# Kernel tuning notes

Hardware: AMD Instinct MI355X
Metric: run time of the kernel (lower is better)

The kernel has to match this reference:

```python
import jax, jax.numpy as jnp
import numpy as np

B, L, DM, DIN, N, R, K, H = 4, 2048, 1024, 2048, 16, 64, 4, 1024
EPS = 1e-5


def setup_inputs() -> dict:
    key = jax.random.key(0)
    ks = jax.random.split(key, 12)
    nrm = lambda k, shp, s=0.02: jax.random.normal(k, shp, jnp.float32) * s
    return dict(
        hidden_states=jax.random.normal(ks[0], (B, L, DM), jnp.float32),
        residual=jax.random.normal(ks[1], (B, L, DM), jnp.float32),
        norm_w=jnp.ones((DM,), jnp.float32),
        in_proj_w=nrm(ks[2], (2 * DIN, DM)),
        conv_w=nrm(ks[3], (DIN, K), 0.2),
        conv_b=jnp.zeros((DIN,), jnp.float32),
        x_proj_w=nrm(ks[4], (R + 2 * N, DIN)),
        dt_proj_w=nrm(ks[5], (DIN, R), 0.1),
        dt_proj_b=jnp.log(jnp.expm1(jnp.full((DIN,), 0.01, jnp.float32))),
        A_log=jnp.log(jnp.tile(jnp.arange(1, N + 1, dtype=jnp.float32), (DIN, 1))),
        D=jnp.ones((DIN,), jnp.float32),
        out_proj_w=nrm(ks[6], (DM, DIN)),
        norm2_w=jnp.ones((DM,), jnp.float32),
        fc1_w=nrm(ks[7], (2 * H, DM)),
        fc2_w=nrm(ks[8], (DM, H)),
    )


def _rmsnorm(x, w):
    return x * jax.lax.rsqrt(jnp.mean(x * x, axis=-1, keepdims=True) + EPS) * w


def _mixer(h, in_proj_w, conv_w, conv_b, x_proj_w, dt_proj_w, dt_proj_b,
           A_log, D, out_proj_w):
    # in_proj -> x, z : (B, L, DIN) each
    xz = jnp.einsum('bld,ed->ble', h, in_proj_w)
    x, z = jnp.split(xz, 2, axis=-1)
    # depthwise causal conv along L
    xc = x.transpose(0, 2, 1)  # (B, DIN, L)
    xc = jax.lax.conv_general_dilated(
        xc, conv_w[:, None, :], window_strides=(1,), padding=[(K - 1, 0)],
        feature_group_count=DIN)
    xc = xc + conv_b[None, :, None]
    x = jax.nn.silu(xc).transpose(0, 2, 1)  # (B, L, DIN)
    # x_proj -> dt_low, B, C
    dbl = jnp.einsum('bld,ed->ble', x, x_proj_w)
    dt_low, Bm, Cm = jnp.split(dbl, [R, R + N], axis=-1)
    dt = jax.nn.softplus(jnp.einsum('blr,dr->bld', dt_low, dt_proj_w) + dt_proj_b)
    A = -jnp.exp(A_log)  # (DIN, N)

    def step(hc, inp):
        dt_t, B_t, C_t, x_t = inp  # (B,DIN),(B,N),(B,N),(B,DIN)
        hc = jnp.exp(dt_t[..., None] * A) * hc + (dt_t * x_t)[..., None] * B_t[:, None, :]
        return hc, jnp.einsum('bdn,bn->bd', hc, C_t)

    h0 = jnp.zeros((B, DIN, N), x.dtype)
    _, ys = jax.lax.scan(step, h0, (dt.transpose(1, 0, 2), Bm.transpose(1, 0, 2),
                                    Cm.transpose(1, 0, 2), x.transpose(1, 0, 2)))
    y = ys.transpose(1, 0, 2) + x * D  # skip term D*u
    y = y * jax.nn.silu(z)
    return jnp.einsum('bld,ed->ble', y, out_proj_w)


def reference(hidden_states, residual, norm_w, in_proj_w, conv_w, conv_b,
              x_proj_w, dt_proj_w, dt_proj_b, A_log, D, out_proj_w,
              norm2_w, fc1_w, fc2_w):
    # pre-norm residual path (fused_add_norm=False, residual_in_fp32=True)
    res = hidden_states + residual
    hn = _rmsnorm(res, norm_w)
    mix = _mixer(hn, in_proj_w, conv_w, conv_b, x_proj_w, dt_proj_w,
                 dt_proj_b, A_log, D, out_proj_w)
    # NOTE: faithful to source: residual is overwritten by norm2(mix+res),
    # while mlp is applied to the raw mixer output.
    res2 = _rmsnorm(mix + res, norm2_w)
    fc = jnp.einsum('bld,hd->blh', mix, fc1_w)
    y, gate = jnp.split(fc, 2, axis=-1)
    out = jnp.einsum('blh,dh->bld', y * jax.nn.silu(gate), fc2_w)
    return (out, res2)
```

## Files before the change

### kernel.cpp

```cpp
#include <hip/hip_runtime.h>
#include <hip/hip_bf16.h>

#define B_   4
#define L_   2048
#define DM_  1024
#define DIN_ 2048
#define NS_  16
#define R_   64
#define KC_  4
#define H_   1024
#define BL_  (B_ * L_)
#define CCH  32
#define CHL  (L_ / CCH)

typedef __attribute__((ext_vector_type(4))) float f32x4;
typedef __attribute__((ext_vector_type(8))) short bf16x8;
typedef __attribute__((ext_vector_type(8))) unsigned short u16x8;

__device__ __forceinline__ float b2f(unsigned short u) {
    union { unsigned int i; float f; } v; v.i = ((unsigned int)u) << 16; return v.f;
}
__device__ __forceinline__ unsigned short f2b(float f) {
    union { float f; unsigned int i; } v; v.f = f;
    unsigned int r = v.i + 0x7fffu + ((v.i >> 16) & 1u);
    return (unsigned short)(r >> 16);
}
__device__ __forceinline__ float sigmoidf_(float x) { return 1.f / (1.f + __expf(-x)); }
__device__ __forceinline__ float softplusf_(float x) { return (x > 20.f) ? x : log1pf(__expf(x)); }

__device__ __forceinline__ void gload16(const unsigned short* g, unsigned short* l) {
    __builtin_amdgcn_global_load_lds(
        (__attribute__((address_space(1))) void*)(g),
        (__attribute__((address_space(3))) void*)(l), 16, 0, 0);
}

__global__ void k_cvt(const float* __restrict__ in, unsigned short* __restrict__ out, int n) {
    int i = blockIdx.x * blockDim.x + threadIdx.x;
    if (i < n) out[i] = f2b(in[i]);
}
__global__ void k_fill0(unsigned short* __restrict__ out, int n) {
    int i = blockIdx.x * blockDim.x + threadIdx.x;
    if (i < n) out[i] = 0;
}

__global__ __launch_bounds__(256)
void k_reduceX(const float* __restrict__ part, unsigned short* __restrict__ dblB,
               float* __restrict__ dblF) {
    int i = blockIdx.x * 256 + threadIdx.x;
    if (i >= BL_ * 96) return;
    int r = i / 96, n = i - r * 96;
    const float* p = part + (size_t)r * 2048;
    float s = p[n] + p[128 + n] + p[256 + n] + p[384 + n];
    dblB[(size_t)r * 96 + n] = f2b(s);
    if (n >= 64) dblF[(size_t)r * 32 + n - 64] = s;
}

__global__ __launch_bounds__(256)
void k_add_rmsnorm(const float* __restrict__ a, const float* __restrict__ b,
                   const float* __restrict__ w,
                   float* __restrict__ resOut, unsigned short* __restrict__ hnOut) {
    int row = blockIdx.x, tid = threadIdx.x;
    const float4* ap = (const float4*)(a + (size_t)row * DM_);
    const float4* bp = (const float4*)(b + (size_t)row * DM_);
    float4 va = ap[tid], vb = bp[tid];
    float4 s = make_float4(va.x + vb.x, va.y + vb.y, va.z + vb.z, va.w + vb.w);
    ((float4*)(resOut + (size_t)row * DM_))[tid] = s;
    float ss = s.x * s.x + s.y * s.y + s.z * s.z + s.w * s.w;
    #pragma unroll
    for (int m = 32; m >= 1; m >>= 1) ss += __shfl_xor(ss, m);
    __shared__ float red[4];
    if ((tid & 63) == 0) red[tid >> 6] = ss;
    __syncthreads();
    float tot = red[0] + red[1] + red[2] + red[3];
    float sc = rsqrtf(tot / (float)DM_ + 1e-5f);
    float4 vw = ((const float4*)w)[tid];
    unsigned short* hp = hnOut + (size_t)row * DM_ + tid * 4;
    *(ushort4*)hp = make_ushort4(f2b(s.x * sc * vw.x), f2b(s.y * sc * vw.y),
                                 f2b(s.z * sc * vw.z), f2b(s.w * sc * vw.w));
}

__global__ __launch_bounds__(256)
void k_add_rmsnorm2(const float* __restrict__ mix, const float* __restrict__ res,
                    const float* __restrict__ w,
                    float* __restrict__ res2Out, unsigned short* __restrict__ mixB) {
    int row = blockIdx.x, tid = threadIdx.x;
    const float4* mp = (const float4*)(mix + (size_t)row * DM_);
    const float4* rp = (const float4*)(res + (size_t)row * DM_);
    float4 vm = mp[tid], vr = rp[tid];
    float4 s = make_float4(vm.x + vr.x, vm.y + vr.y, vm.z + vr.z, vm.w + vr.w);
    unsigned short* mb = mixB + (size_t)row * DM_ + tid * 4;
    *(ushort4*)mb = make_ushort4(f2b(vm.x), f2b(vm.y), f2b(vm.z), f2b(vm.w));
    float ss = s.x * s.x + s.y * s.y + s.z * s.z + s.w * s.w;
    #pragma unroll
    for (int m = 32; m >= 1; m >>= 1) ss += __shfl_xor(ss, m);
    __shared__ float red[4];
    if ((tid & 63) == 0) red[tid >> 6] = ss;
    __syncthreads();
    float tot = red[0] + red[1] + red[2] + red[3];
    float sc = rsqrtf(tot / (float)DM_ + 1e-5f);
    float4 vw = ((const float4*)w)[tid];
    float4 o = make_float4(s.x * sc * vw.x, s.y * sc * vw.y, s.z * sc * vw.z, s.w * sc * vw.w);
    ((float4*)(res2Out + (size_t)row * DM_))[tid] = o;
}

__global__ __launch_bounds__(256)
void k_conv_silu(const unsigned short* __restrict__ xz,
                 const float* __restrict__ cw, const float* __restrict__ cb,
                 unsigned short* __restrict__ xc) {
    const int tid = threadIdx.x;
    const int d0 = tid * 8;
    const int b  = blockIdx.x >> 8;
    const int t0 = (blockIdx.x & 255) * 8;
    const unsigned short* xbase = xz + (size_t)b * L_ * (2 * DIN_) + d0;
    unsigned short* obase = xc + (size_t)b * L_ * DIN_ + d0;

    float4 w[8];
    float bias[8];
    #pragma unroll
    for (int j = 0; j < 8; j++) {
        w[j] = ((const float4*)cw)[d0 + j];
        bias[j] = cb[d0 + j];
    }
    u16x8 zero = (u16x8){0, 0, 0, 0, 0, 0, 0, 0};
    u16x8 r0 = zero, r1 = zero, r2 = zero, r3;
    if (t0 >= 3) {
        r0 = *(const u16x8*)(xbase + (size_t)(t0 - 3) * (2 * DIN_));
        r1 = *(const u16x8*)(xbase + (size_t)(t0 - 2) * (2 * DIN_));
        r2 = *(const u16x8*)(xbase + (size_t)(t0 - 1) * (2 * DIN_));
    }
    #pragma unroll
    for (int tt = 0; tt < 8; tt++) {
        int t = t0 + tt;
        r3 = *(const u16x8*)(xbase + (size_t)t * (2 * DIN_));
        u16x8 out;
        #pragma unroll
        for (int j = 0; j < 8; j++) {
            float acc = bias[j] + w[j].x * b2f(r0[j]) + w[j].y * b2f(r1[j])
                                + w[j].z * b2f(r2[j]) + w[j].w * b2f(r3[j]);
            out[j] = f2b(acc * sigmoidf_(acc));
        }
        *(u16x8*)(obase + (size_t)t * DIN_) = out;
        r0 = r1; r1 = r2; r2 = r3;
    }
}

__global__ void k_gate(const unsigned short* __restrict__ fc, unsigned short* __restrict__ g) {
    int i = blockIdx.x * blockDim.x + threadIdx.x;
    if (i >= BL_ * H_) return;
    int h = i % H_;
    int row = i / H_;
    float y = b2f(fc[(size_t)row * (2 * H_) + h]);
    float gt = b2f(fc[(size_t)row * (2 * H_) + H_ + h]);
    g[i] = f2b(y * gt * sigmoidf_(gt));
}

__global__ __launch_bounds__(256)
void k_scan_p1(const unsigned short* __restrict__ dty, const unsigned short* __restrict__ xc,
               const float* __restrict__ dblF, const float* __restrict__ A_log,
               unsigned short* __restrict__ Q, unsigned short* __restrict__ sumdt) {
    const int tid = threadIdx.x;
    const int d = (blockIdx.x & 7) * 256 + tid;
    const int b = blockIdx.x >> 3;
    const int c = blockIdx.y;
    const int t0 = c * CHL;

    float a[NS_], h[NS_];
    #pragma unroll
    for (int n = 0; n < NS_; n++) { a[n] = -__expf(A_log[d * NS_ + n]); h[n] = 0.f; }
    float sd = 0.f;

    const unsigned short* dp  = dty + (size_t)b * L_ * DIN_ + d;
    const unsigned short* xp  = xc  + (size_t)b * L_ * DIN_ + d;
    const float* bcp = dblF + (size_t)(b * L_ + t0) * 32;

    #pragma unroll 2
    for (int t = 0; t < CHL; t++) {
        int tg = t0 + t;
        float dtv = b2f(dp[(size_t)tg * DIN_]);
        float xv  = b2f(xp[(size_t)tg * DIN_]);
        sd += dtv;
        float bx = dtv * xv;
        const float* bc = bcp + t * 32;
        #pragma unroll
        for (int n = 0; n < NS_; n++)
            h[n] = __expf(dtv * a[n]) * h[n] + bx * bc[n];
    }
    unsigned short* q = Q + ((size_t)(b * CCH + c) * DIN_ + d) * NS_;
    u16x8 qa, qb;
    #pragma unroll
    for (int j = 0; j < 8; j++) { qa[j] = f2b(h[j]); qb[j] = f2b(h[8 + j]); }
    *(u16x8*)q = qa;
    *(u16x8*)(q + 8) = qb;
    sumdt[(size_t)(b * CCH + c) * DIN_ + d] = f2b(sd);
}

__global__ __launch_bounds__(256)
void k_scan_comb(unsigned short* __restrict__ Q, const unsigned short* __restrict__ sumdt,
                 const float* __restrict__ A_log) {
    int i = blockIdx.x * 256 + threadIdx.x;
    int n = i & 15;
    int d = (i >> 4) & (DIN_ - 1);
    int b = i >> 15;
    float a = -__expf(A_log[d * NS_ + n]);
    float h = 0.f;
    for (int c = 0; c < CCH; c++) {
        size_t base = ((size_t)(b * CCH + c) * DIN_ + d);
        float q  = b2f(Q[base * NS_ + n]);
        float sd = b2f(sumdt[base]);
        if (c > 0) Q[((size_t)(b * CCH + c - 1) * DIN_ + d) * NS_ + n] = f2b(h);
        h = __expf(a * sd) * h + q;
    }
}

__global__ __launch_bounds__(256)
void k_scan_p3(unsigned short* __restrict__ dty, const unsigned short* __restrict__ xc,
               const float* __restrict__ dblF, const float* __restrict__ A_log,
               const float* __restrict__ Dp, const unsigned short* __restrict__ xz,
               const unsigned short* __restrict__ Qh) {
    const int tid = threadIdx.x;
    const int d = (blockIdx.x & 7) * 256 + tid;
    const int b = blockIdx.x >> 3;
    const int c = blockIdx.y;
    const int t0 = c * CHL;

    float a[NS_], h[NS_];
    #pragma unroll
    for (int n = 0; n < NS_; n++) a[n] = -__expf(A_log[d * NS_ + n]);
    if (c == 0) {
        #pragma unroll
        for (int n = 0; n < NS_; n++) h[n] = 0.f;
    } else {
        const unsigned short* qh = Qh + ((size_t)(b * CCH + c - 1) * DIN_ + d) * NS_;
        u16x8 v0 = *(const u16x8*)qh;
        u16x8 v1 = *(const u16x8*)(qh + 8);
        #pragma unroll
        for (int j = 0; j < 8; j++) { h[j] = b2f(v0[j]); h[8 + j] = b2f(v1[j]); }
    }
    float Dd = Dp[d];

    unsigned short* dp = dty + (size_t)b * L_ * DIN_ + d;
    const unsigned short* xp  = xc + (size_t)b * L_ * DIN_ + d;
    const unsigned short* zp  = xz + (size_t)b * L_ * (2 * DIN_) + DIN_ + d;
    const float* bcp = dblF + (size_t)(b * L_ + t0) * 32;

    #pragma unroll 2
    for (int t = 0; t < CHL; t++) {
        int tg = t0 + t;
        float dtv = b2f(dp[(size_t)tg * DIN_]);
        float xv  = b2f(xp[(size_t)tg * DIN_]);
        float bx = dtv * xv;
        const float* bc = bcp + t * 32;
        float y = 0.f;
        #pragma unroll
        for (int n = 0; n < NS_; n++) {
            h[n] = __expf(dtv * a[n]) * h[n] + bx * bc[n];
            y += h[n] * bc[16 + n];
        }
        y += xv * Dd;
        float zv = b2f(zp[(size_t)tg * (2 * DIN_)]);
        dp[(size_t)tg * DIN_] = f2b(y * zv * sigmoidf_(zv));
    }
}

template <int EPI, int SPLITK = 0>
__global__ __launch_bounds__(256)
void k_gemm(const unsigned short* __restrict__ A, int lda,
            const unsigned short* __restrict__ Bw, int ldb,
            void* __restrict__ outp, int ldc, const float* __restrict__ bias,
            int M, int N, int Kd, int Nstore) {
    if constexpr (SPLITK) {
        const int z = blockIdx.z;
        A += (size_t)z * 512;
        Bw += (size_t)z * 512;
        outp = (void*)((float*)outp + z * 128);
    }
    __shared__ unsigned short As[128 * 32];
    __shared__ unsigned short Bs[128 * 32];
    const int tid = threadIdx.x;
    const int lane = tid & 63;
    const int w = tid >> 6;
    const int wr = w >> 1, wc = w & 1;
    const int bm = blockIdx.y * 128, bn = blockIdx.x * 128;

    const int e0 = tid * 8;
    const int r0 = e0 >> 5;
    const int c0 = e0 & 31;
    const int r1 = r0 + 64;

    f32x4 acc[4][4];
    #pragma unroll
    for (int i = 0; i < 4; i++)
        #pragma unroll
        for (int j = 0; j < 4; j++) acc[i][j] = (f32x4){0.f, 0.f, 0.f, 0.f};

    const int fr = lane & 15, ko = (lane >> 4) * 8;

    for (int k0 = 0; k0 < Kd; k0 += 32) {
        gload16(A  + (size_t)(bm + r0) * lda + k0 + c0, &As[e0]);
        gload16(A  + (size_t)(bm + r1) * lda + k0 + c0, &As[e0 + 2048]);
        gload16(Bw + (size_t)(bn + r0) * ldb + k0 + c0, &Bs[e0]);
        gload16(Bw + (size_t)(bn + r1) * ldb + k0 + c0, &Bs[e0 + 2048]);
        __syncthreads();
        bf16x8 af[4], bv[4];
        #pragma unroll
        for (int i = 0; i < 4; i++)
            af[i] = *(const bf16x8*)&As[(wr * 64 + i * 16 + fr) * 32 + ko];
        #pragma unroll
        for (int j = 0; j < 4; j++)
            bv[j] = *(const bf16x8*)&Bs[(wc * 64 + j * 16 + fr) * 32 + ko];
        #pragma unroll
        for (int i = 0; i < 4; i++)
            #pragma unroll
            for (int j = 0; j < 4; j++)
                acc[i][j] = __builtin_amdgcn_mfma_f32_16x16x32_bf16(af[i], bv[j], acc[i][j], 0, 0, 0);
        __syncthreads();
    }

    const int rr = (lane >> 4) * 4;
    const int cc = lane & 15;
    #pragma unroll
    for (int i = 0; i < 4; i++) {
        #pragma unroll
        for (int j = 0; j < 4; j++) {
            int col = bn + wc * 64 + j * 16 + cc;
            if (col >= Nstore) continue;
            #pragma unroll
            for (int q = 0; q < 4; q++) {
                int row = bm + wr * 64 + i * 16 + rr + q;
                float v = acc[i][j][q];
                if constexpr (EPI == 2) { v += bias[col]; v = softplusf_(v); }
                if constexpr (EPI == 0)
                    ((float*)outp)[(size_t)row * ldc + col] = v;
                else
                    ((unsigned short*)outp)[(size_t)row * ldc + col] = f2b(v);
            }
        }
    }
}

#define SBAR   __builtin_amdgcn_s_barrier()
#define SCHED0 __builtin_amdgcn_sched_barrier(0)
#define SLOT(r) ((((r) ^ ((r) >> 2)) & 3) << 4)

template <int EPI, int BN>
__global__ __launch_bounds__(512, 2)
void k_gemm256(const unsigned short* __restrict__ Aptr, int lda,
               const unsigned short* __restrict__ Bptr, int ldb,
               void* __restrict__ outp, int ldc, int Kd) {
    extern __shared__ unsigned short lds[];
    constexpr int WN = BN / 64;
    constexpr int MF = (BN == 256) ? 8 : 4;
    constexpr int BSL = BN * 32;
    constexpr int BBASE = 32768;
    const int tid  = threadIdx.x;
    const int lane = tid & 63;
    const int wid  = tid >> 6;
    const int wr = wid / WN, wc = wid % WN;
    const int bm = blockIdx.y * 256, bn = blockIdx.x * BN;
    const int fr = lane & 15, sk = lane >> 4;

    f32x4 acc[MF][4];
    #pragma unroll
    for (int i = 0; i < MF; i++)
        #pragma unroll
        for (int j = 0; j < 4; j++) acc[i][j] = (f32x4){0.f, 0.f, 0.f, 0.f};

    const int NT = Kd >> 6;

    const int o0 = tid * 16, o1 = (512 + tid) * 16;
    const int sr0 = o0 >> 6, sr1 = o1 >> 6;
    const int sc0 = (o0 & 63) ^ SLOT(sr0);
    const int sc1 = (o1 & 63) ^ SLOT(sr1);
    const unsigned short* Ag0 = Aptr + (size_t)(bm + sr0) * lda + (sc0 >> 1);
    const unsigned short* Ag1 = Aptr + (size_t)(bm + sr1) * lda + (sc1 >> 1);
    const unsigned short* Bg0 = Bptr + (size_t)(bn + sr0) * ldb + (sc0 >> 1);
    const unsigned short* Bg1 = Bptr + (size_t)(bn + sr1) * ldb + (sc1 >> 1);
    unsigned short* LA0 = lds + (o0 >> 1);
    unsigned short* LA1 = lds + (o1 >> 1);
    unsigned short* LB0 = lds + BBASE + (o0 >> 1);
    unsigned short* LB1 = lds + BBASE + (o1 >> 1);

    auto stageA = [&](int buf, int ks, int kt) {
        int s = (buf * 2 + ks) * 8192;
        gload16(Ag0 + kt * 64 + ks * 32, LA0 + s);
        gload16(Ag1 + kt * 64 + ks * 32, LA1 + s);
    };
    auto stageB = [&](int buf, int ks, int kt) {
        int s = (buf * 2 + ks) * BSL;
        gload16(Bg0 + kt * 64 + ks * 32, LB0 + s);
        if constexpr (BN == 256) gload16(Bg1 + kt * 64 + ks * 32, LB1 + s);
    };

    const int rsw  = (sk * 16) ^ SLOT(fr);
    const int aoff = (wr * (MF * 16) + fr) * 32 + (rsw >> 1);
    const int boff = (wc * 64 + fr) * 32 + (rsw >> 1);

#define DSREAD_B(buf, ks) { _Pragma("unroll") for (int n = 0; n < 4; n++) \
    bv[n] = *(const bf16x8*)&lds[BBASE + ((buf)*2+(ks))*BSL + boff + n*512]; }
#define DSREAD_A4(buf, ks, mh) { _Pragma("unroll") for (int m = 0; m < 4; m++) \
    af[m] = *(const bf16x8*)&lds[((buf)*2+(ks))*8192 + aoff + ((mh)*4+m)*512]; }
#define MFMA16(mh) { __builtin_amdgcn_s_setprio(1); \
    _Pragma("unroll") for (int m = 0; m < 4; m++) \
      _Pragma("unroll") for (int n = 0; n < 4; n++) \
        acc[(mh)*4+m][n] = __builtin_amdgcn_mfma_f32_16x16x32_bf16(af[m], bv[n], acc[(mh)*4+m][n], 0, 0, 0); \
    __builtin_amdgcn_s_setprio(0); }

    if constexpr (BN == 256) {
        stageA(0, 0, 0); stageB(0, 0, 0); stageA(0, 1, 0); stageB(0, 1, 0);
        SCHED0;
        asm volatile("s_waitcnt vmcnt(4)" ::: "memory");
        SBAR;

        int buf = 0;
        for (int kt = 0; kt < NT - 1; ++kt) {
            bf16x8 af[4], bv[4];
            DSREAD_B(buf, 0); DSREAD_A4(buf, 0, 0);
            stageA(buf ^ 1, 0, kt + 1);
            SCHED0; SBAR;
            MFMA16(0);
            SCHED0; SBAR;
            DSREAD_A4(buf, 0, 1);
            stageB(buf ^ 1, 0, kt + 1);
            SCHED0; SBAR;
            MFMA16(1);
            SCHED0;
            asm volatile("s_waitcnt vmcnt(4)" ::: "memory");
            SBAR;
            DSREAD_B(buf, 1); DSREAD_A4(buf, 1, 0);
            stageA(buf ^ 1, 1, kt + 1);
            SCHED0; SBAR;
            MFMA16(0);
            SCHED0; SBAR;
            DSREAD_A4(buf, 1, 1);
            stageB(buf ^ 1, 1, kt + 1);
            SCHED0; SBAR;
            MFMA16(1);
            SCHED0;
            asm volatile("s_waitcnt vmcnt(4)" ::: "memory");
            SBAR;
            buf ^= 1;
        }
        {
            bf16x8 af[4], bv[4];
            DSREAD_B(buf, 0); DSREAD_A4(buf, 0, 0);
            SCHED0; SBAR;
            MFMA16(0);
            SCHED0; SBAR;
            DSREAD_A4(buf, 0, 1);
            SCHED0; SBAR;
            MFMA16(1);
            SCHED0;
            asm volatile("s_waitcnt vmcnt(0)" ::: "memory");
            SBAR;
            DSREAD_B(buf, 1); DSREAD_A4(buf, 1, 0);
            SCHED0; SBAR;
            MFMA16(0);
            SCHED0; SBAR;
            DSREAD_A4(buf, 1, 1);
            SCHED0; SBAR;
            MFMA16(1);
        }
    } else {
        stageA(0, 0, 0); stageB(0, 0, 0); stageA(0, 1, 0); stageB(0, 1, 0);
        SCHED0;
        asm volatile("s_waitcnt vmcnt(3)" ::: "memory");
        SBAR;

        int buf = 0;
        for (int kt = 0; kt < NT - 1; ++kt) {
            bf16x8 af[4], bv[4];
            DSREAD_B(buf, 0); DSREAD_A4(buf, 0, 0);
            stageA(buf ^ 1, 0, kt + 1); stageB(buf ^ 1, 0, kt + 1);
            SCHED0; SBAR;
            MFMA16(0);
            SCHED0;
            asm volatile("s_waitcnt vmcnt(3)" ::: "memory");
            SBAR;
            DSREAD_B(buf, 1); DSREAD_A4(buf, 1, 0);
            stageA(buf ^ 1, 1, kt + 1); stageB(buf ^ 1, 1, kt + 1);
            SCHED0; SBAR;
            MFMA16(0);
            SCHED0;
            asm volatile("s_waitcnt vmcnt(3)" ::: "memory");
            SBAR;
            buf ^= 1;
        }
        {
            bf16x8 af[4], bv[4];
            DSREAD_B(buf, 0); DSREAD_A4(buf, 0, 0);
            SCHED0; SBAR;
            MFMA16(0);
            SCHED0;
            asm volatile("s_waitcnt vmcnt(0)" ::: "memory");
            SBAR;
            DSREAD_B(buf, 1); DSREAD_A4(buf, 1, 0);
            SCHED0; SBAR;
            MFMA16(0);
        }
    }
#undef DSREAD_B
#undef DSREAD_A4
#undef MFMA16

    const int rr = sk * 4;
    const int cc = fr;
    #pragma unroll
    for (int mf = 0; mf < MF; mf++) {
        #pragma unroll
        for (int nf = 0; nf < 4; nf++) {
            int col = bn + wc * 64 + nf * 16 + cc;
            #pragma unroll
            for (int q = 0; q < 4; q++) {
                int row = bm + wr * (MF * 16) + mf * 16 + rr + q;
                float v = acc[mf][nf][q];
                if constexpr (EPI == 0)
                    ((float*)outp)[(size_t)row * ldc + col] = v;
                else
                    ((unsigned short*)outp)[(size_t)row * ldc + col] = f2b(v);
            }
        }
    }
}

extern "C" void kernel_launch(void* const* d_in, const int* in_sizes, int n_in,
                              void* d_out, int out_size, void* d_ws, size_t ws_size,
                              hipStream_t stream) {
    const float* hs        = (const float*)d_in[0];
    const float* resi      = (const float*)d_in[1];
    const float* norm_w    = (const float*)d_in[2];
    const float* in_proj_w = (const float*)d_in[3];
    const float* conv_w    = (const float*)d_in[4];
    const float* conv_b    = (const float*)d_in[5];
    const float* x_proj_w  = (const float*)d_in[6];
    const float* dt_proj_w = (const float*)d_in[7];
    const float* dt_proj_b = (const float*)d_in[8];
    const float* A_log     = (const float*)d_in[9];
    const float* Dp        = (const float*)d_in[10];
    const float* out_proj_w= (const float*)d_in[11];
    const float* norm2_w   = (const float*)d_in[12];
    const float* fc1_w     = (const float*)d_in[13];
    const float* fc2_w     = (const float*)d_in[14];

    static bool attrDone = false;
    if (!attrDone) {
        hipFuncSetAttribute(reinterpret_cast<const void*>(k_gemm256<0, 256>),
                            hipFuncAttributeMaxDynamicSharedMemorySize, 131072);
        hipFuncSetAttribute(reinterpret_cast<const void*>(k_gemm256<1, 256>),
                            hipFuncAttributeMaxDynamicSharedMemorySize, 131072);
        hipFuncSetAttribute(reinterpret_cast<const void*>(k_gemm256<0, 128>),
                            hipFuncAttributeMaxDynamicSharedMemorySize, 98304);
        attrDone = true;
    }

    char* ws = (char*)d_ws;
    size_t off = 0;
    auto alloc = [&](size_t bytes) {
        void* p = ws + off;
        off = (off + bytes + 255) & ~(size_t)255;
        return p;
    };

    unsigned short* xzB  = (unsigned short*)alloc((size_t)BL_ * 2 * DIN_ * 2);
    unsigned short* fcB  = xzB;
    unsigned short* gB   = xzB + (size_t)BL_ * 2 * H_;
    unsigned short* mixB = gB  + (size_t)BL_ * H_;
    void* S_xc = alloc((size_t)BL_ * DIN_ * 2);
    unsigned short* hnB    = (unsigned short*)S_xc;
    unsigned short* xconvB = (unsigned short*)S_xc;
    float*          mixF   = (float*)S_xc;
    unsigned short* dblB = (unsigned short*)alloc((size_t)BL_ * 96 * 2);
    unsigned short* inprojB  = (unsigned short*)alloc((size_t)2 * DIN_ * DM_ * 2);
    unsigned short* xprojB   = (unsigned short*)alloc((size_t)128 * DIN_ * 2);
    unsigned short* dtprojB  = (unsigned short*)alloc((size_t)DIN_ * R_ * 2);
    unsigned short* outprojB = (unsigned short*)alloc((size_t)DM_ * DIN_ * 2);
    unsigned short* fc1B     = (unsigned short*)alloc((size_t)2 * H_ * DM_ * 2);
    unsigned short* fc2B     = (unsigned short*)alloc((size_t)DM_ * H_ * 2);
    float*          dblF     = (float*)alloc((size_t)BL_ * 32 * 4);

    unsigned short* scanQ  = inprojB;
    unsigned short* scanSd = xprojB;

    float* outMain = (float*)d_out;
    float* outRes2 = (float*)d_out + (size_t)BL_ * DM_;
    float*          resF = outMain;
    unsigned short* dtyB = (unsigned short*)outRes2;

    {
        int n;
        n = 2 * DIN_ * DM_; k_cvt<<<(n + 255) / 256, 256, 0, stream>>>(in_proj_w, inprojB, n);
        n = 96 * DIN_;      k_cvt<<<(n + 255) / 256, 256, 0, stream>>>(x_proj_w, xprojB, n);
        n = 32 * DIN_;      k_fill0<<<(n + 255) / 256, 256, 0, stream>>>(xprojB + 96 * DIN_, n);
        n = DIN_ * R_;      k_cvt<<<(n + 255) / 256, 256, 0, stream>>>(dt_proj_w, dtprojB, n);
        n = DM_ * DIN_;     k_cvt<<<(n + 255) / 256, 256, 0, stream>>>(out_proj_w, outprojB, n);
        n = 2 * H_ * DM_;   k_cvt<<<(n + 255) / 256, 256, 0, stream>>>(fc1_w, fc1B, n);
        n = DM_ * H_;       k_cvt<<<(n + 255) / 256, 256, 0, stream>>>(fc2_w, fc2B, n);
    }

    k_add_rmsnorm<<<BL_, 256, 0, stream>>>(hs, resi, norm_w, resF, hnB);

    k_gemm256<1, 256><<<dim3(2 * DIN_ / 256, BL_ / 256), 512, 131072, stream>>>(
        hnB, DM_, inprojB, DM_, (void*)xzB, 2 * DIN_, DM_);

    k_conv_silu<<<B_ * 256, 256, 0, stream>>>(xzB, conv_w, conv_b, xconvB);

    k_gemm<0, 1><<<dim3(1, BL_ / 128, 4), 256, 0, stream>>>(
        xconvB, DIN_, xprojB, DIN_, (void*)(float*)xzB, 2048, nullptr, BL_, 128, 512, 128);

    k_reduceX<<<(BL_ * 96 + 255) / 256, 256, 0, stream>>>((const float*)xzB, dblB, dblF);

    k_gemm<2><<<dim3(DIN_ / 128, BL_ / 128), 256, 0, stream>>>(
        dblB, 96, dtprojB, R_, (void*)dtyB, DIN_, dt_proj_b, BL_, DIN_, R_, DIN_);

    k_scan_p1<<<dim3(B_ * (DIN_ / 256), CCH), 256, 0, stream>>>(
        dtyB, xconvB, dblF, A_log, scanQ, scanSd);
    k_scan_comb<<<(B_ * DIN_ * NS_) / 256, 256, 0, stream>>>(scanQ, scanSd, A_log);
    k_scan_p3<<<dim3(B_ * (DIN_ / 256), CCH), 256, 0, stream>>>(
        dtyB, xconvB, dblF, A_log, Dp, xzB, scanQ);

    k_gemm256<0, 128><<<dim3(DM_ / 128, BL_ / 256), 512, 98304, stream>>>(
        dtyB, DIN_, outprojB, DIN_, (void*)mixF, DM_, DIN_);

    k_add_rmsnorm2<<<BL_, 256, 0, stream>>>(mixF, resF, norm2_w, outRes2, mixB);

    k_gemm256<1, 256><<<dim3(2 * H_ / 256, BL_ / 256), 512, 131072, stream>>>(
        mixB, DM_, fc1B, DM_, (void*)fcB, 2 * H_, DM_);

    k_gate<<<(BL_ * H_ + 255) / 256, 256, 0, stream>>>(fcB, gB);

    k_gemm256<0, 128><<<dim3(DM_ / 128, BL_ / 256), 512, 98304, stream>>>(
        gB, H_, fc2B, H_, (void*)outMain, DM_, H_);
}
```

Baseline: 501.3 us.

## Vectorize elementwise kernels, use exp2 in scan, swizzle GEMM blocks, more scan chunks

Several unrelated changes land together. The weight-conversion and gate kernels now use vector loads and stores, and the scan uses exp2 with A pre-scaled by log2(e). The 256-row GEMM gets an XCD-aware block swizzle, and the chunked scan doubles its chunk count to 64 when workspace allows. Together these target memory-bound elementwise overhead, scan ALU cost, cache locality across chiplets, and scan parallelism, at the cost of more carry-combine work and extra workspace.

```diff
diff --git a/kernel.cpp b/kernel.cpp
--- a/kernel.cpp
+++ b/kernel.cpp
@@ -10,12 +10,17 @@
 #define KC_  4
 #define H_   1024
 #define BL_  (B_ * L_)
-#define CCH  32
-#define CHL  (L_ / CCH)
 
 typedef __attribute__((ext_vector_type(4))) float f32x4;
 typedef __attribute__((ext_vector_type(8))) short bf16x8;
 typedef __attribute__((ext_vector_type(8))) unsigned short u16x8;
+
+#if __has_builtin(__builtin_amdgcn_exp2f)
+#define EXP2(x) __builtin_amdgcn_exp2f(x)
+#else
+#define EXP2(x) exp2f(x)
+#endif
+#define LOG2E 1.44269504088896f
 
 __device__ __forceinline__ float b2f(unsigned short u) {
     union { unsigned int i; float f; } v; v.i = ((unsigned int)u) << 16; return v.f;
@@ -34,13 +39,16 @@
         (__attribute__((address_space(3))) void*)(l), 16, 0, 0);
 }
 
-__global__ void k_cvt(const float* __restrict__ in, unsigned short* __restrict__ out, int n) {
+__global__ void k_cvt4(const float* __restrict__ in, unsigned short* __restrict__ out, int n4) {
     int i = blockIdx.x * blockDim.x + threadIdx.x;
-    if (i < n) out[i] = f2b(in[i]);
-}
-__global__ void k_fill0(unsigned short* __restrict__ out, int n) {
+    if (i < n4) {
+        float4 v = ((const float4*)in)[i];
+        ((ushort4*)out)[i] = make_ushort4(f2b(v.x), f2b(v.y), f2b(v.z), f2b(v.w));
+    }
+}
+__global__ void k_fill04(unsigned short* __restrict__ out, int n4) {
     int i = blockIdx.x * blockDim.x + threadIdx.x;
-    if (i < n) out[i] = 0;
+    if (i < n4) ((ushort4*)out)[i] = make_ushort4(0, 0, 0, 0);
 }
 
 __global__ __launch_bounds__(256)
@@ -144,29 +152,36 @@
     }
 }
 
-__global__ void k_gate(const unsigned short* __restrict__ fc, unsigned short* __restrict__ g) {
-    int i = blockIdx.x * blockDim.x + threadIdx.x;
-    if (i >= BL_ * H_) return;
-    int h = i % H_;
-    int row = i / H_;
-    float y = b2f(fc[(size_t)row * (2 * H_) + h]);
-    float gt = b2f(fc[(size_t)row * (2 * H_) + H_ + h]);
-    g[i] = f2b(y * gt * sigmoidf_(gt));
-}
-
+__global__ __launch_bounds__(256)
+void k_gate(const unsigned short* __restrict__ fc, unsigned short* __restrict__ g) {
+    int i = blockIdx.x * 256 + threadIdx.x;
+    int row = i >> 7;
+    int h8 = (i & 127) * 8;
+    u16x8 y8 = *(const u16x8*)(fc + (size_t)row * (2 * H_) + h8);
+    u16x8 g8 = *(const u16x8*)(fc + (size_t)row * (2 * H_) + H_ + h8);
+    u16x8 o;
+    #pragma unroll
+    for (int j = 0; j < 8; j++) {
+        float y = b2f(y8[j]), gt = b2f(g8[j]);
+        o[j] = f2b(y * gt * sigmoidf_(gt));
+    }
+    *(u16x8*)(g + (size_t)row * H_ + h8) = o;
+}
+
+template <int CHLT>
 __global__ __launch_bounds__(256)
 void k_scan_p1(const unsigned short* __restrict__ dty, const unsigned short* __restrict__ xc,
                const float* __restrict__ dblF, const float* __restrict__ A_log,
-               unsigned short* __restrict__ Q, unsigned short* __restrict__ sumdt) {
+               unsigned short* __restrict__ Q, unsigned short* __restrict__ sumdt, int cch) {
     const int tid = threadIdx.x;
     const int d = (blockIdx.x & 7) * 256 + tid;
     const int b = blockIdx.x >> 3;
     const int c = blockIdx.y;
-    const int t0 = c * CHL;
+    const int t0 = c * CHLT;
 
     float a[NS_], h[NS_];
     #pragma unroll
-    for (int n = 0; n < NS_; n++) { a[n] = -__expf(A_log[d * NS_ + n]); h[n] = 0.f; }
+    for (int n = 0; n < NS_; n++) { a[n] = -__expf(A_log[d * NS_ + n]) * LOG2E; h[n] = 0.f; }
     float sd = 0.f;
 
     const unsigned short* dp  = dty + (size_t)b * L_ * DIN_ + d;
@@ -174,7 +189,7 @@
     const float* bcp = dblF + (size_t)(b * L_ + t0) * 32;
 
     #pragma unroll 2
-    for (int t = 0; t < CHL; t++) {
+    for (int t = 0; t < CHLT; t++) {
         int tg = t0 + t;
         float dtv = b2f(dp[(size_t)tg * DIN_]);
         float xv  = b2f(xp[(size_t)tg * DIN_]);
@@ -183,54 +198,55 @@
         const float* bc = bcp + t * 32;
         #pragma unroll
         for (int n = 0; n < NS_; n++)
-            h[n] = __expf(dtv * a[n]) * h[n] + bx * bc[n];
-    }
-    unsigned short* q = Q + ((size_t)(b * CCH + c) * DIN_ + d) * NS_;
+            h[n] = EXP2(dtv * a[n]) * h[n] + bx * bc[n];
+    }
+    unsigned short* q = Q + ((size_t)(b * cch + c) * DIN_ + d) * NS_;
     u16x8 qa, qb;
     #pragma unroll
     for (int j = 0; j < 8; j++) { qa[j] = f2b(h[j]); qb[j] = f2b(h[8 + j]); }
     *(u16x8*)q = qa;
     *(u16x8*)(q + 8) = qb;
-    sumdt[(size_t)(b * CCH + c) * DIN_ + d] = f2b(sd);
+    sumdt[(size_t)(b * cch + c) * DIN_ + d] = f2b(sd);
 }
 
 __global__ __launch_bounds__(256)
 void k_scan_comb(unsigned short* __restrict__ Q, const unsigned short* __restrict__ sumdt,
-                 const float* __restrict__ A_log) {
+                 const float* __restrict__ A_log, int cch) {
     int i = blockIdx.x * 256 + threadIdx.x;
     int n = i & 15;
     int d = (i >> 4) & (DIN_ - 1);
     int b = i >> 15;
-    float a = -__expf(A_log[d * NS_ + n]);
+    float a = -__expf(A_log[d * NS_ + n]) * LOG2E;
     float h = 0.f;
-    for (int c = 0; c < CCH; c++) {
-        size_t base = ((size_t)(b * CCH + c) * DIN_ + d);
+    for (int c = 0; c < cch; c++) {
+        size_t base = ((size_t)(b * cch + c) * DIN_ + d);
         float q  = b2f(Q[base * NS_ + n]);
         float sd = b2f(sumdt[base]);
-        if (c > 0) Q[((size_t)(b * CCH + c - 1) * DIN_ + d) * NS_ + n] = f2b(h);
-        h = __expf(a * sd) * h + q;
-    }
-}
-
+        if (c > 0) Q[((size_t)(b * cch + c - 1) * DIN_ + d) * NS_ + n] = f2b(h);
+        h = EXP2(a * sd) * h + q;
+    }
+}
+
+template <int CHLT>
 __global__ __launch_bounds__(256)
 void k_scan_p3(unsigned short* __restrict__ dty, const unsigned short* __restrict__ xc,
                const float* __restrict__ dblF, const float* __restrict__ A_log,
                const float* __restrict__ Dp, const unsigned short* __restrict__ xz,
-               const unsigned short* __restrict__ Qh) {
+               const unsigned short* __restrict__ Qh, int cch) {
     const int tid = threadIdx.x;
     const int d = (blockIdx.x & 7) * 256 + tid;
     const int b = blockIdx.x >> 3;
     const int c = blockIdx.y;
-    const int t0 = c * CHL;
+    const int t0 = c * CHLT;
 
     float a[NS_], h[NS_];
     #pragma unroll
-    for (int n = 0; n < NS_; n++) a[n] = -__expf(A_log[d * NS_ + n]);
+    for (int n = 0; n < NS_; n++) a[n] = -__expf(A_log[d * NS_ + n]) * LOG2E;
     if (c == 0) {
         #pragma unroll
         for (int n = 0; n < NS_; n++) h[n] = 0.f;
     } else {
-        const unsigned short* qh = Qh + ((size_t)(b * CCH + c - 1) * DIN_ + d) * NS_;
+        const unsigned short* qh = Qh + ((size_t)(b * cch + c - 1) * DIN_ + d) * NS_;
         u16x8 v0 = *(const u16x8*)qh;
         u16x8 v1 = *(const u16x8*)(qh + 8);
         #pragma unroll
@@ -244,7 +260,7 @@
     const float* bcp = dblF + (size_t)(b * L_ + t0) * 32;
 
     #pragma unroll 2
-    for (int t = 0; t < CHL; t++) {
+    for (int t = 0; t < CHLT; t++) {
         int tg = t0 + t;
         float dtv = b2f(dp[(size_t)tg * DIN_]);
         float xv  = b2f(xp[(size_t)tg * DIN_]);
@@ -253,7 +269,7 @@
         float y = 0.f;
         #pragma unroll
         for (int n = 0; n < NS_; n++) {
-            h[n] = __expf(dtv * a[n]) * h[n] + bx * bc[n];
+            h[n] = EXP2(dtv * a[n]) * h[n] + bx * bc[n];
             y += h[n] * bc[16 + n];
         }
         y += xv * Dd;
@@ -356,7 +372,14 @@
     const int lane = tid & 63;
     const int wid  = tid >> 6;
     const int wr = wid / WN, wc = wid % WN;
-    const int bm = blockIdx.y * 256, bn = blockIdx.x * BN;
+
+    const int gdx = (int)gridDim.x;
+    const int nwg = gdx * (int)gridDim.y;
+    const int orig = (int)blockIdx.y * gdx + (int)blockIdx.x;
+    const int cpx = nwg >> 3;
+    const int swz = (orig & 7) * cpx + (orig >> 3);
+    const int bm = (swz / gdx) * 256, bn = (swz % gdx) * BN;
+
     const int fr = lane & 15, sk = lane >> 4;
 
     f32x4 acc[MF][4];
@@ -577,8 +600,21 @@
     unsigned short* fc2B     = (unsigned short*)alloc((size_t)DM_ * H_ * 2);
     float*          dblF     = (float*)alloc((size_t)BL_ * 32 * 4);
 
-    unsigned short* scanQ  = inprojB;
-    unsigned short* scanSd = xprojB;
+    unsigned short *scanQ, *scanSd;
+    int cch;
+    {
+        size_t needQ  = (size_t)B_ * 64 * DIN_ * NS_ * 2;
+        size_t needSd = (size_t)B_ * 64 * DIN_ * 2;
+        if (ws_size >= off + needQ + needSd + 512) {
+            scanQ  = (unsigned short*)alloc(needQ);
+            scanSd = (unsigned short*)alloc(needSd);
+            cch = 64;
+        } else {
+            scanQ  = inprojB;
+            scanSd = xprojB;
+            cch = 32;
+        }
+    }
 
     float* outMain = (float*)d_out;
     float* outRes2 = (float*)d_out + (size_t)BL_ * DM_;
@@ -587,13 +623,13 @@
 
     {
         int n;
-        n = 2 * DIN_ * DM_; k_cvt<<<(n + 255) / 256, 256, 0, stream>>>(in_proj_w, inprojB, n);
-        n = 96 * DIN_;      k_cvt<<<(n + 255) / 256, 256, 0, stream>>>(x_proj_w, xprojB, n);
-        n = 32 * DIN_;      k_fill0<<<(n + 255) / 256, 256, 0, stream>>>(xprojB + 96 * DIN_, n);
-        n = DIN_ * R_;      k_cvt<<<(n + 255) / 256, 256, 0, stream>>>(dt_proj_w, dtprojB, n);
-        n = DM_ * DIN_;     k_cvt<<<(n + 255) / 256, 256, 0, stream>>>(out_proj_w, outprojB, n);
-        n = 2 * H_ * DM_;   k_cvt<<<(n + 255) / 256, 256, 0, stream>>>(fc1_w, fc1B, n);
-        n = DM_ * H_;       k_cvt<<<(n + 255) / 256, 256, 0, stream>>>(fc2_w, fc2B, n);
+        n = 2 * DIN_ * DM_ / 4; k_cvt4<<<(n + 255) / 256, 256, 0, stream>>>(in_proj_w, inprojB, n);
+        n = 96 * DIN_ / 4;      k_cvt4<<<(n + 255) / 256, 256, 0, stream>>>(x_proj_w, xprojB, n);
+        n = 32 * DIN_ / 4;      k_fill04<<<(n + 255) / 256, 256, 0, stream>>>(xprojB + 96 * DIN_, n);
+        n = DIN_ * R_ / 4;      k_cvt4<<<(n + 255) / 256, 256, 0, stream>>>(dt_proj_w, dtprojB, n);
+        n = DM_ * DIN_ / 4;     k_cvt4<<<(n + 255) / 256, 256, 0, stream>>>(out_proj_w, outprojB, n);
+        n = 2 * H_ * DM_ / 4;   k_cvt4<<<(n + 255) / 256, 256, 0, stream>>>(fc1_w, fc1B, n);
+        n = DM_ * H_ / 4;       k_cvt4<<<(n + 255) / 256, 256, 0, stream>>>(fc2_w, fc2B, n);
     }
 
     k_add_rmsnorm<<<BL_, 256, 0, stream>>>(hs, resi, norm_w, resF, hnB);
@@ -611,11 +647,19 @@
     k_gemm<2><<<dim3(DIN_ / 128, BL_ / 128), 256, 0, stream>>>(
         dblB, 96, dtprojB, R_, (void*)dtyB, DIN_, dt_proj_b, BL_, DIN_, R_, DIN_);
 
-    k_scan_p1<<<dim3(B_ * (DIN_ / 256), CCH), 256, 0, stream>>>(
-        dtyB, xconvB, dblF, A_log, scanQ, scanSd);
-    k_scan_comb<<<(B_ * DIN_ * NS_) / 256, 256, 0, stream>>>(scanQ, scanSd, A_log);
-    k_scan_p3<<<dim3(B_ * (DIN_ / 256), CCH), 256, 0, stream>>>(
-        dtyB, xconvB, dblF, A_log, Dp, xzB, scanQ);
+    if (cch == 64) {
+        k_scan_p1<32><<<dim3(B_ * (DIN_ / 256), 64), 256, 0, stream>>>(
+            dtyB, xconvB, dblF, A_log, scanQ, scanSd, 64);
+        k_scan_comb<<<(B_ * DIN_ * NS_) / 256, 256, 0, stream>>>(scanQ, scanSd, A_log, 64);
+        k_scan_p3<32><<<dim3(B_ * (DIN_ / 256), 64), 256, 0, stream>>>(
+            dtyB, xconvB, dblF, A_log, Dp, xzB, scanQ, 64);
+    } else {
+        k_scan_p1<64><<<dim3(B_ * (DIN_ / 256), 32), 256, 0, stream>>>(
+            dtyB, xconvB, dblF, A_log, scanQ, scanSd, 32);
+        k_scan_comb<<<(B_ * DIN_ * NS_) / 256, 256, 0, stream>>>(scanQ, scanSd, A_log, 32);
+        k_scan_p3<64><<<dim3(B_ * (DIN_ / 256), 32), 256, 0, stream>>>(
+            dtyB, xconvB, dblF, A_log, Dp, xzB, scanQ, 32);
+    }
 
     k_gemm256<0, 128><<<dim3(DM_ / 128, BL_ / 256), 512, 98304, stream>>>(
         dtyB, DIN_, outprojB, DIN_, (void*)mixF, DM_, DIN_);
@@ -625,7 +669,7 @@
     k_gemm256<1, 256><<<dim3(2 * H_ / 256, BL_ / 256), 512, 131072, stream>>>(
         mixB, DM_, fc1B, DM_, (void*)fcB, 2 * H_, DM_);
 
-    k_gate<<<(BL_ * H_ + 255) / 256, 256, 0, stream>>>(fcB, gB);
+    k_gate<<<(BL_ * H_ / 8) / 256, 256, 0, stream>>>(fcB, gB);
 
     k_gemm256<0, 128><<<dim3(DM_ / 128, BL_ / 256), 512, 98304, stream>>>(
         gB, H_, fc2B, H_, (void*)outMain, DM_, H_);
```

After: 475.7 us. 5.1% less time.
